# Performance work log

Measured on AMD Instinct MI355X. Metric: run time of the kernel, lower is better.

The kernel has to match this reference:

```python
import jax, jax.numpy as jnp
import numpy as np

B, LQ, E, R, H = 4, 64, 512, 32, 768
HOP = 2

def _linear(x, W, b):
    return x @ W + b

def setup_inputs() -> dict:
    key = jax.random.key(0)
    ks = jax.random.split(key, 20)
    s = 0.02
    inp = {
        'question_embedding': jax.random.normal(ks[0], (B, LQ, H), jnp.float32),
        'question_mask': jnp.ones((B, LQ), jnp.float32),
        'entity_embedding': jax.random.normal(ks[1], (B, E, H), jnp.float32),
        'rel_embedding': jax.random.normal(ks[2], (B, E, R, H), jnp.float32),
        'adj': jax.random.randint(ks[3], (B, E, R), 0, E, jnp.int32),
        'node_mask': jax.random.bernoulli(ks[4], 0.95, (B, E)).astype(jnp.float32),
        'adj_mask': jax.random.bernoulli(ks[5], 0.9, (B, E, R)).astype(jnp.float32),
        # params (Linear: y = x @ W + b, W is [in, out])
        'proj_W': jax.random.normal(ks[6], (H, H), jnp.float32) * s,
        'proj_b': jnp.zeros((H,), jnp.float32),
        'rproj_W': jax.random.normal(ks[7], (H, H), jnp.float32) * s,
        'rproj_b': jnp.zeros((H,), jnp.float32),
        'msg_W': jax.random.normal(ks[8], (HOP, 2 * H, H), jnp.float32) * s,
        'msg_b': jnp.zeros((HOP, H), jnp.float32),
        'upd_W': jax.random.normal(ks[9], (HOP, 2 * H, H), jnp.float32) * s,
        'upd_b': jnp.zeros((HOP, H), jnp.float32),
        'relscore_W': jax.random.normal(ks[10], (2 * H, 1), jnp.float32) * s,
        'relscore_b': jnp.zeros((1,), jnp.float32),
        'score_W': jax.random.normal(ks[11], (H, 1), jnp.float32) * s,
        'score_b': jnp.zeros((1,), jnp.float32),
    }
    return inp

def reference(question_embedding, question_mask, entity_embedding, rel_embedding,
              adj, node_mask, adj_mask,
              proj_W, proj_b, rproj_W, rproj_b, msg_W, msg_b, upd_W, upd_b,
              relscore_W, relscore_b, score_W, score_b):
    gelu = lambda x: jax.nn.gelu(x, approximate=False)  # torch nn.GELU default is erf
    dtype = rel_embedding.dtype
    NEG = jnp.finfo(dtype).min

    qe = _linear(question_embedding, proj_W, proj_b)          # [B,LQ,H]
    ee = _linear(entity_embedding, proj_W, proj_b)            # [B,E,H]
    re = _linear(rel_embedding, rproj_W, rproj_b)             # [B,E,R,H]

    qm = question_mask[..., None]
    q = jnp.sum(qe * qm, axis=1) / jnp.sum(qm, axis=1)        # [B,H]

    weight_mask = (1.0 - adj_mask) * NEG                      # [B,E,R]
    q_exp = jnp.broadcast_to(q[:, None, None, :], (B, E, R, H))
    weight_logit = (_linear(jnp.concatenate([re, q_exp], -1), relscore_W, relscore_b)
                    .squeeze(-1) + weight_mask)               # [B,E,R]
    weight = adj_mask * jax.nn.softmax(weight_logit, axis=-1) # [B,E,R]

    adj_flat = adj.reshape(B, E * R)
    for k in range(HOP):
        tail = jnp.take_along_axis(ee, adj_flat[:, :, None], axis=1).reshape(B, E, R, H)
        messages = gelu(_linear(jnp.concatenate([re, tail], -1), msg_W[k], msg_b[k]))
        agg = jnp.einsum('berh,ber->beh', messages, weight)
        ee = gelu(_linear(jnp.concatenate([ee, agg], -1), upd_W[k], upd_b[k]))

    node_neg = (1.0 - node_mask[..., None]) * NEG
    ent_score = (_linear(ee, score_W, score_b) + node_neg).squeeze(-1)  # [B,E]

    # triple_sim (computed under no_grad in torch)
    ee_c = jax.lax.stop_gradient(ee)
    q_c = jax.lax.stop_gradient(q)
    q_source = jnp.einsum('bh,beh->be', q_c, ee_c)            # source node e repeated over R
    q_source = jnp.broadcast_to(q_source[:, :, None], (B, E, R)).reshape(B, E * R)
    tail_final = jnp.take_along_axis(ee_c, adj_flat[:, :, None], axis=1)
    q_target = jnp.einsum('bh,bnh->bn', q_c, tail_final)      # [B,E*R]
    triple_sim = q_source + q_target + jax.lax.stop_gradient(weight_logit).reshape(B, E * R)

    return (ee, ent_score, weight_logit, triple_sim)
```

## Files before the change

### kernel.cpp

```cpp
#include <hip/hip_runtime.h>

#define NEGF (-3.0e38f)

#define BB 4
#define LQQ 64
#define EE_N 512
#define RR 32
#define HH 768

#define WS_QBAR 0
#define WS_Q    3072
#define WS_QD   6144
#define WS_WR1C 6656
#define WS_D0   7424
#define WS_D1   8192
#define WS_C0   8960
#define WS_C1   598784
#define WS_EEA  1188608
#define WS_EEB  2761472
#define WS_EEW  4334336
#define WS_W    5907200
#define WS_AGG  5972736
#define WS_SDOT 7545600
#define WS_CKT0 7547648
#define WS_CKT1 7842560
#define WS_PWT  8137472
#define WS_W0BT 8432384
#define WS_W1BT 8727296
#define WS_U0TT 9022208
#define WS_U0BT 9317120
#define WS_U1TT 9612032
#define WS_U1BT 9906944
#define WS_M0TT 10201856
#define WS_M1TT 10496768

typedef __attribute__((ext_vector_type(8))) short short8v;
typedef __attribute__((ext_vector_type(4))) short short4v;
typedef __attribute__((ext_vector_type(4))) float f32x4;

__device__ __forceinline__ float gelu_erf(float x) {
    return 0.5f * x * (1.0f + erff(x * 0.70710678118654752f));
}

__device__ __forceinline__ unsigned short f2bf(float f) {
    unsigned int u = __float_as_uint(f);
    unsigned int r = (u + 0x7fffu + ((u >> 16) & 1u)) >> 16;
    return (unsigned short)r;
}

__device__ __forceinline__ float bf2f(unsigned short h) {
    return __uint_as_float(((unsigned int)h) << 16);
}

__global__ void k_qbar(const float* __restrict__ QE, const float* __restrict__ QM,
                       float* __restrict__ qbar) {
    int b = blockIdx.x;
    int tid = threadIdx.x;
    float msum = 0.f;
    for (int l = 0; l < LQQ; ++l) msum += QM[b*LQQ + l];
    for (int h = tid; h < HH; h += 256) {
        float s = 0.f;
        for (int l = 0; l < LQQ; ++l)
            s += QM[b*LQQ + l] * QE[((size_t)(b*LQQ + l))*HH + h];
        qbar[b*HH + h] = s / msum;
    }
}

__global__ void k_small2(const float* __restrict__ RW, const float* __restrict__ RB,
                         const float* __restrict__ RSW, const float* __restrict__ RSB,
                         const float* __restrict__ q, float* __restrict__ wr1c,
                         float* __restrict__ qd) {
    const int wid = threadIdx.x >> 6, lane = threadIdx.x & 63;
    const int blk = blockIdx.x;
    if (blk < 192) {
        int row = blk*4 + wid;
        const float* a = RW + (size_t)row*HH;
        float acc = 0.f;
        #pragma unroll
        for (int p = 0; p < 3; ++p) {
            int i4 = (p*64 + lane) << 2;
            float4 x = *(const float4*)(a + i4);
            float4 w = *(const float4*)(RSW + i4);
            acc += x.x*w.x + x.y*w.y + x.z*w.z + x.w*w.w;
        }
        for (int off = 32; off; off >>= 1) acc += __shfl_xor(acc, off);
        if (lane == 0) wr1c[row] = acc;
    } else {
        float acc = 0.f, acc2 = 0.f;
        const float* src = q + wid*HH;
        #pragma unroll
        for (int p = 0; p < 3; ++p) {
            int i4 = (p*64 + lane) << 2;
            float4 x = *(const float4*)(src + i4);
            float4 w = *(const float4*)(RSW + HH + i4);
            acc += x.x*w.x + x.y*w.y + x.z*w.z + x.w*w.w;
            if (wid == 0) {
                float4 rb = *(const float4*)(RB + i4);
                float4 w0 = *(const float4*)(RSW + i4);
                acc2 += rb.x*w0.x + rb.y*w0.y + rb.z*w0.z + rb.w*w0.w;
            }
        }
        for (int off = 32; off; off >>= 1) { acc += __shfl_xor(acc, off); acc2 += __shfl_xor(acc2, off); }
        if (lane == 0) qd[wid] = acc;
        if (wid == 0 && lane == 0) qd[BB] = acc2 + RSB[0];
    }
}

__global__ void k_dk2(const unsigned short* __restrict__ M0tT,
                      const unsigned short* __restrict__ M1tT,
                      const float* __restrict__ RB, const float* __restrict__ MB,
                      float* __restrict__ d0, float* __restrict__ d1) {
    const int gw = blockIdx.x*4 + (threadIdx.x >> 6);
    const int lane = threadIdx.x & 63;
    const int hop = gw >= HH;
    const int n = hop ? gw - HH : gw;
    const unsigned short* row = (hop ? M1tT : M0tT) + (size_t)n*HH;
    float s = 0.f;
    #pragma unroll
    for (int p = 0; p < 3; ++p) {
        int i4 = (p*64 + lane) << 2;
        const unsigned short* hp = row + i4;
        float4 rv = *(const float4*)(RB + i4);
        s += bf2f(hp[0])*rv.x + bf2f(hp[1])*rv.y + bf2f(hp[2])*rv.z + bf2f(hp[3])*rv.w;
    }
    for (int off = 32; off; off >>= 1) s += __shfl_xor(s, off);
    if (lane == 0) (hop ? d1 : d0)[n] = s + MB[hop*HH + n];
}

__global__ __launch_bounds__(256) void gemm_f32(
    const float* __restrict__ A1, const float* __restrict__ W1,
    const float* __restrict__ bias, float* __restrict__ C,
    int M, int N, int K, int act)
{
    __shared__ float Asm[16][68];
    __shared__ float Bs[16][68];
    const int tid = threadIdx.x;
    const int n0 = blockIdx.x * 64;
    const int m0 = blockIdx.y * 64;
    const int tm = tid >> 4;
    const int tn = tid & 15;
    float acc[4][4] = {};
    for (int kk = 0; kk < K; kk += 16) {
        const int ar = tid >> 2;
        const int ak = (tid & 3) << 2;
        float4 av = make_float4(0.f, 0.f, 0.f, 0.f);
        if (m0 + ar < M) av = *(const float4*)(A1 + (size_t)(m0 + ar)*K + kk + ak);
        const int br = tid >> 4;
        const int bc = (tid & 15) << 2;
        float4 bv = *(const float4*)(W1 + (size_t)(kk + br)*N + n0 + bc);
        __syncthreads();
        Asm[ak+0][ar] = av.x; Asm[ak+1][ar] = av.y;
        Asm[ak+2][ar] = av.z; Asm[ak+3][ar] = av.w;
        *(float4*)&Bs[br][bc] = bv;
        __syncthreads();
        #pragma unroll
        for (int k = 0; k < 16; ++k) {
            float4 a4 = *(const float4*)&Asm[k][tm << 2];
            float4 b4 = *(const float4*)&Bs[k][tn << 2];
            float a[4] = {a4.x, a4.y, a4.z, a4.w};
            float b[4] = {b4.x, b4.y, b4.z, b4.w};
            #pragma unroll
            for (int i = 0; i < 4; ++i)
                #pragma unroll
                for (int j = 0; j < 4; ++j)
                    acc[i][j] = fmaf(a[i], b[j], acc[i][j]);
        }
    }
    float4 bb = make_float4(0.f, 0.f, 0.f, 0.f);
    if (bias) bb = *(const float4*)(bias + n0 + (tn << 2));
    float bbv[4] = {bb.x, bb.y, bb.z, bb.w};
    #pragma unroll
    for (int i = 0; i < 4; ++i) {
        int m = m0 + (tm << 2) + i;
        if (m >= M) break;
        #pragma unroll
        for (int j = 0; j < 4; ++j) {
            float v = acc[i][j] + bbv[j];
            if (act) v = gelu_erf(v);
            C[(size_t)m*N + n0 + (tn << 2) + j] = v;
        }
    }
}

__global__ void k_ckt(const float* __restrict__ Ck, unsigned short* __restrict__ CkT) {
    __shared__ float t[32][33];
    const int k0 = blockIdx.x * 32, n0 = blockIdx.y * 32;
    const int tid = threadIdx.x;
    {
        int r = tid >> 3;
        int c4 = (tid & 7) << 2;
        float4 v = *(const float4*)(Ck + (size_t)(k0 + r)*HH + n0 + c4);
        t[r][c4+0] = v.x; t[r][c4+1] = v.y; t[r][c4+2] = v.z; t[r][c4+3] = v.w;
    }
    __syncthreads();
    {
        int n = tid >> 3;
        int k4 = (tid & 7) << 2;
        unsigned short o[4];
        #pragma unroll
        for (int j = 0; j < 4; ++j) o[j] = f2bf(t[k4+j][n]);
        *(uint2*)(CkT + (size_t)(n0 + n)*HH + k0 + k4) = *(const uint2*)o;
    }
}

struct WPairs { const float* s[9]; unsigned short* d[9]; };
__global__ void k_w2bf(WPairs p) {
    __shared__ float t[32][33];
    const float* __restrict__ Ck = p.s[blockIdx.z];
    unsigned short* __restrict__ CkT = p.d[blockIdx.z];
    const int k0 = blockIdx.x * 32, n0 = blockIdx.y * 32;
    const int tid = threadIdx.x;
    {
        int r = tid >> 3;
        int c4 = (tid & 7) << 2;
        float4 v = *(const float4*)(Ck + (size_t)(k0 + r)*HH + n0 + c4);
        t[r][c4+0] = v.x; t[r][c4+1] = v.y; t[r][c4+2] = v.z; t[r][c4+3] = v.w;
    }
    __syncthreads();
    {
        int n = tid >> 3;
        int k4 = (tid & 7) << 2;
        unsigned short o[4];
        #pragma unroll
        for (int j = 0; j < 4; ++j) o[j] = f2bf(t[k4+j][n]);
        *(uint2*)(CkT + (size_t)(n0 + n)*HH + k0 + k4) = *(const uint2*)o;
    }
}

template<int BM>
__global__ __launch_bounds__(256) void gemm_bf16(
    const float* __restrict__ A1, const unsigned short* __restrict__ W1T,
    const float* __restrict__ A2, const unsigned short* __restrict__ W2T,
    const float* __restrict__ bias, float* __restrict__ C, int act)
{
    constexpr int FM = BM / 32;
    constexpr int AC = BM / 16;
    __shared__ alignas(16) unsigned short As[BM*64];
    __shared__ alignas(16) unsigned short Bs[128*64];
    const int tid = threadIdx.x;
    const int n0 = blockIdx.x * 128;
    const int m0 = blockIdx.y * BM;
    const int w = tid >> 6, lane = tid & 63;
    const int wm = w >> 1, wn = w & 1;
    const int l15 = lane & 15, l4 = lane >> 4;
    const int am_row = tid >> 4;
    const int am_col = (tid & 15) * 4;
    const int bm_row = tid >> 3;
    const int bm_col = (tid & 7) * 8;
    f32x4 acc[FM][4];
    #pragma unroll
    for (int i = 0; i < FM; ++i)
        #pragma unroll
        for (int j = 0; j < 4; ++j) acc[i][j] = (f32x4){0.f,0.f,0.f,0.f};
    const int nPass = (A2 != nullptr) ? 2 : 1;
    for (int pass = 0; pass < nPass; ++pass) {
        const float* __restrict__ A = pass ? A2 : A1;
        const unsigned short* __restrict__ WT = pass ? W2T : W1T;
        for (int k0 = 0; k0 < HH; k0 += 64) {
            float4 av[AC];
            #pragma unroll
            for (int c = 0; c < AC; ++c)
                av[c] = *(const float4*)(A + (size_t)(m0 + c*16 + am_row)*HH + k0 + am_col);
            short8v bv[4];
            #pragma unroll
            for (int i = 0; i < 4; ++i)
                bv[i] = *(const short8v*)(WT + (size_t)(n0 + i*32 + bm_row)*HH + k0 + bm_col);
            __syncthreads();
            #pragma unroll
            for (int c = 0; c < AC; ++c) {
                int r = c*16 + am_row;
                short4v h;
                h[0]=(short)f2bf(av[c].x); h[1]=(short)f2bf(av[c].y);
                h[2]=(short)f2bf(av[c].z); h[3]=(short)f2bf(av[c].w);
                int ba = r*128 + ((am_col*2) ^ ((r & 7) << 4));
                *(short4v*)&As[ba >> 1] = h;
            }
            #pragma unroll
            for (int i = 0; i < 4; ++i) {
                int r = i*32 + bm_row;
                int ba = r*128 + ((bm_col*2) ^ ((r & 7) << 4));
                *(short8v*)&Bs[ba >> 1] = bv[i];
            }
            __syncthreads();
            #pragma unroll
            for (int ks = 0; ks < 2; ++ks) {
                const int kb = ks*64 + l4*16;
                short8v af[FM], bf[4];
                #pragma unroll
                for (int fm = 0; fm < FM; ++fm) {
                    int row = wm*(FM*16) + fm*16 + l15;
                    af[fm] = *(const short8v*)&As[(row*128 + (kb ^ ((row & 7) << 4))) >> 1];
                }
                #pragma unroll
                for (int fn = 0; fn < 4; ++fn) {
                    int row = wn*64 + fn*16 + l15;
                    bf[fn] = *(const short8v*)&Bs[(row*128 + (kb ^ ((row & 7) << 4))) >> 1];
                }
                #pragma unroll
                for (int fm = 0; fm < FM; ++fm)
                    #pragma unroll
                    for (int fn = 0; fn < 4; ++fn)
                        acc[fm][fn] = __builtin_amdgcn_mfma_f32_16x16x32_bf16(af[fm], bf[fn], acc[fm][fn], 0, 0, 0);
            }
            __syncthreads();
        }
    }
    #pragma unroll
    for (int fn = 0; fn < 4; ++fn) {
        int col = n0 + wn*64 + fn*16 + l15;
        float bb = bias ? bias[col] : 0.f;
        #pragma unroll
        for (int fm = 0; fm < FM; ++fm) {
            int row0 = m0 + wm*(FM*16) + fm*16 + l4*4;
            #pragma unroll
            for (int j = 0; j < 4; ++j) {
                float v = acc[fm][fn][j] + bb;
                if (act) v = gelu_erf(v);
                C[(size_t)(row0 + j)*HH + col] = v;
            }
        }
    }
}

template<int FUSE>
__global__ __launch_bounds__(256, 3) void k_msg6(
    const float* __restrict__ rel, const unsigned short* __restrict__ CkT,
    const float* __restrict__ dk, const float* __restrict__ eeW,
    const float* __restrict__ weight_in, const int* __restrict__ adj,
    const float* __restrict__ wr1c, const float* __restrict__ qd,
    const float* __restrict__ am,
    float* __restrict__ agg, float* __restrict__ logit_out,
    float* __restrict__ weight_out)
{
    __shared__ alignas(16) unsigned short As[64*64];
    __shared__ alignas(16) unsigned short Bs[256*64];
    int*   adjS = (int*)As;
    float* wS   = (float*)(As + 128);
    float* lgS  = (float*)(As + 256);
    const int tid = threadIdx.x;
    const int bid = blockIdx.x;
    const int L = (bid & 7) * 384 + (bid >> 3);
    const int mt = L / 3, nt = L - mt*3;
    const int n0 = nt * 256;
    const int m0 = mt * 64;
    const int be0 = mt * 2;
    const int b = be0 >> 9;
    const int wn = tid >> 6, lane = tid & 63;
    const int l15 = lane & 15, l4 = lane >> 4;
    const int am_row = tid >> 4;
    const int am_col = (tid & 15) * 4;
    const int bm_row = tid >> 3;
    const int bm_col = (tid & 7) * 8;
    const float* apA = rel + (size_t)(m0 + am_row)*HH + am_col;
    const unsigned short* apB = CkT + (size_t)(n0 + bm_row)*HH + bm_col;

    f32x4 acc[4][4];
    #pragma unroll
    for (int i = 0; i < 4; ++i)
        #pragma unroll
        for (int j = 0; j < 4; ++j) acc[i][j] = (f32x4){0.f,0.f,0.f,0.f};
    float lg[4] = {0.f, 0.f, 0.f, 0.f};

    float4 av[4];
    short8v bv[8];
    #pragma unroll
    for (int c = 0; c < 4; ++c) av[c] = *(const float4*)(apA + (size_t)c*16*HH);
    #pragma unroll
    for (int i = 0; i < 8; ++i) bv[i] = *(const short8v*)(apB + (size_t)i*32*HH);

    for (int t = 0; t < 12; ++t) {
        const int k0 = t*64;
        #pragma unroll
        for (int c = 0; c < 4; ++c) {
            int r = c*16 + am_row;
            short4v h;
            h[0]=(short)f2bf(av[c].x); h[1]=(short)f2bf(av[c].y);
            h[2]=(short)f2bf(av[c].z); h[3]=(short)f2bf(av[c].w);
            int ba = r*128 + ((am_col*2) ^ ((r & 7) << 4));
            *(short4v*)&As[ba >> 1] = h;
        }
        #pragma unroll
        for (int i = 0; i < 8; ++i) {
            int r = i*32 + bm_row;
            int ba = r*128 + ((bm_col*2) ^ ((r & 7) << 4));
            *(short8v*)&Bs[ba >> 1] = bv[i];
        }
        if (FUSE) {
            float4 wv = *(const float4*)(wr1c + k0 + am_col);
            #pragma unroll
            for (int c = 0; c < 4; ++c)
                lg[c] += av[c].x*wv.x + av[c].y*wv.y + av[c].z*wv.z + av[c].w*wv.w;
        }
        if (t < 11) {
            #pragma unroll
            for (int c = 0; c < 4; ++c)
                av[c] = *(const float4*)(apA + (size_t)c*16*HH + k0 + 64);
            #pragma unroll
            for (int i = 0; i < 8; ++i)
                bv[i] = *(const short8v*)(apB + (size_t)i*32*HH + k0 + 64);
        }
        __syncthreads();
        #pragma unroll
        for (int ks = 0; ks < 2; ++ks) {
            const int kb = ks*64 + l4*16;
            short8v af[4], bf[4];
            #pragma unroll
            for (int fm = 0; fm < 4; ++fm) {
                int row = fm*16 + l15;
                af[fm] = *(const short8v*)&As[(row*128 + (kb ^ ((row & 7) << 4))) >> 1];
            }
            #pragma unroll
            for (int fn = 0; fn < 4; ++fn) {
                int row = wn*64 + fn*16 + l15;
                bf[fn] = *(const short8v*)&Bs[(row*128 + (kb ^ ((row & 7) << 4))) >> 1];
            }
            #pragma unroll
            for (int fm = 0; fm < 4; ++fm)
                #pragma unroll
                for (int fn = 0; fn < 4; ++fn)
                    acc[fm][fn] = __builtin_amdgcn_mfma_f32_16x16x32_bf16(af[fm], bf[fn], acc[fm][fn], 0, 0, 0);
        }
        __syncthreads();
    }
    if (tid < 64) adjS[tid] = adj[be0*RR + tid];
    if (!FUSE && tid < 64) wS[tid] = weight_in[be0*RR + tid];

    if (FUSE) {
        #pragma unroll
        for (int c = 0; c < 4; ++c) {
            lg[c] += __shfl_xor(lg[c], 1);
            lg[c] += __shfl_xor(lg[c], 2);
            lg[c] += __shfl_xor(lg[c], 4);
            lg[c] += __shfl_xor(lg[c], 8);
        }
        if ((tid & 15) == 0) {
            #pragma unroll
            for (int c = 0; c < 4; ++c) lgS[c*16 + am_row] = lg[c];
        }
        __syncthreads();
        if (tid < 64) {
            int r = tid & 31;
            float amv = am[be0*RR + tid];
            float l = lgS[tid] + qd[b] + qd[BB] + (1.0f - amv) * NEGF;
            float mx = l;
            #pragma unroll
            for (int off = 16; off; off >>= 1) mx = fmaxf(mx, __shfl_xor(mx, off, 32));
            float e = expf(l - mx);
            float sm = e;
            #pragma unroll
            for (int off = 16; off; off >>= 1) sm += __shfl_xor(sm, off, 32);
            float wgt = amv * e / sm;
            wS[tid] = wgt;
            if (nt == 0) {
                logit_out[be0*RR + tid] = l;
                weight_out[be0*RR + tid] = wgt;
            }
            (void)r;
        }
    }
    __syncthreads();

    #pragma unroll
    for (int eh = 0; eh < 2; ++eh) {
        const int be = be0 + eh;
        #pragma unroll
        for (int fn = 0; fn < 4; ++fn) {
            int col = n0 + wn*64 + fn*16 + l15;
            float d = dk[col];
            float s = 0.f;
            #pragma unroll
            for (int fp = 0; fp < 2; ++fp) {
                const int fm = eh*2 + fp;
                #pragma unroll
                for (int j = 0; j < 4; ++j) {
                    int rr = fp*16 + l4*4 + j;
                    int t = adjS[eh*RR + rr];
                    float tail = eeW[((size_t)(b*EE_N + t))*HH + col];
                    s += wS[eh*RR + rr] * gelu_erf(acc[fm][fn][j] + tail + d);
                }
            }
            s += __shfl_xor(s, 16);
            s += __shfl_xor(s, 32);
            if (l4 == 0) agg[(size_t)be*HH + col] = s;
        }
    }
}

__global__ __launch_bounds__(256) void k_score(const float* __restrict__ ee,
                                               const float* __restrict__ SW,
                                               const float* __restrict__ SB,
                                               const float* __restrict__ NM,
                                               const float* __restrict__ q,
                                               float* __restrict__ score,
                                               float* __restrict__ sdot) {
    const int wid = threadIdx.x >> 6, lane = threadIdx.x & 63;
    const int row = blockIdx.x*4 + wid;
    const int b = row >> 9;
    const float* er = ee + (size_t)row*HH;
    const float* qr = q + b*HH;
    float a1 = 0.f, a2 = 0.f;
    #pragma unroll
    for (int p = 0; p < 3; ++p) {
        int i4 = (p*64 + lane) << 2;
        float4 e4 = *(const float4*)(er + i4);
        float4 s4 = *(const float4*)(SW + i4);
        float4 q4 = *(const float4*)(qr + i4);
        a1 += e4.x*s4.x + e4.y*s4.y + e4.z*s4.z + e4.w*s4.w;
        a2 += e4.x*q4.x + e4.y*q4.y + e4.z*q4.z + e4.w*q4.w;
    }
    for (int off = 32; off; off >>= 1) { a1 += __shfl_xor(a1, off); a2 += __shfl_xor(a2, off); }
    if (lane == 0) {
        score[row] = a1 + SB[0] + (1.0f - NM[row]) * NEGF;
        sdot[row] = a2;
    }
}

__global__ void k_triple(const float* __restrict__ sdot, const int* __restrict__ adj,
                         const float* __restrict__ logit, float* __restrict__ tri) {
    int idx = blockIdx.x*256 + threadIdx.x;
    int b = idx >> 14;
    int n = idx & 16383;
    int e = n >> 5;
    int a = adj[idx];
    tri[idx] = sdot[b*EE_N + e] + sdot[b*EE_N + a] + logit[idx];
}

extern "C" void kernel_launch(void* const* d_in, const int* in_sizes, int n_in,
                              void* d_out, int out_size, void* d_ws, size_t ws_size,
                              hipStream_t stream) {
    const float* QE  = (const float*)d_in[0];
    const float* QM  = (const float*)d_in[1];
    const float* ENT = (const float*)d_in[2];
    const float* REL = (const float*)d_in[3];
    const int*   ADJ = (const int*)d_in[4];
    const float* NM  = (const float*)d_in[5];
    const float* AM  = (const float*)d_in[6];
    const float* PW  = (const float*)d_in[7];
    const float* PB  = (const float*)d_in[8];
    const float* RW  = (const float*)d_in[9];
    const float* RB  = (const float*)d_in[10];
    const float* MW  = (const float*)d_in[11];
    const float* MB  = (const float*)d_in[12];
    const float* UW  = (const float*)d_in[13];
    const float* UB  = (const float*)d_in[14];
    const float* RSW = (const float*)d_in[15];
    const float* RSB = (const float*)d_in[16];
    const float* SW  = (const float*)d_in[17];
    const float* SB  = (const float*)d_in[18];

    float* out = (float*)d_out;
    float* ws  = (float*)d_ws;
    float* o_ee    = out;
    float* o_score = out + 1572864;
    float* o_logit = out + 1574912;
    float* o_tri   = out + 1640448;

    unsigned short* CkT0 = (unsigned short*)(ws + WS_CKT0);
    unsigned short* CkT1 = (unsigned short*)(ws + WS_CKT1);
    unsigned short* PWT  = (unsigned short*)(ws + WS_PWT);
    unsigned short* W0bT = (unsigned short*)(ws + WS_W0BT);
    unsigned short* W1bT = (unsigned short*)(ws + WS_W1BT);
    unsigned short* U0tT = (unsigned short*)(ws + WS_U0TT);
    unsigned short* U0bT = (unsigned short*)(ws + WS_U0BT);
    unsigned short* U1tT = (unsigned short*)(ws + WS_U1TT);
    unsigned short* U1bT = (unsigned short*)(ws + WS_U1BT);
    unsigned short* M0tT = (unsigned short*)(ws + WS_M0TT);
    unsigned short* M1tT = (unsigned short*)(ws + WS_M1TT);

    const size_t HT = (size_t)2*HH*HH;
    const size_t BOT = (size_t)HH*HH;

    k_qbar<<<BB, 256, 0, stream>>>(QE, QM, ws + WS_QBAR);
    gemm_f32<<<dim3(12,1), 256, 0, stream>>>(ws + WS_QBAR, PW, PB, ws + WS_Q, BB, HH, HH, 0);
    k_small2<<<193, 256, 0, stream>>>(RW, RB, RSW, RSB, ws + WS_Q, ws + WS_WR1C, ws + WS_QD);

    WPairs wp;
    wp.s[0] = PW;            wp.d[0] = PWT;
    wp.s[1] = MW + BOT;      wp.d[1] = W0bT;
    wp.s[2] = MW + HT + BOT; wp.d[2] = W1bT;
    wp.s[3] = UW;            wp.d[3] = U0tT;
    wp.s[4] = UW + BOT;      wp.d[4] = U0bT;
    wp.s[5] = UW + HT;       wp.d[5] = U1tT;
    wp.s[6] = UW + HT + BOT; wp.d[6] = U1bT;
    wp.s[7] = MW;            wp.d[7] = M0tT;
    wp.s[8] = MW + HT;       wp.d[8] = M1tT;
    k_w2bf<<<dim3(24,24,9), 256, 0, stream>>>(wp);

    k_dk2<<<384, 256, 0, stream>>>(M0tT, M1tT, RB, MB, ws + WS_D0, ws + WS_D1);

    gemm_bf16<32><<<dim3(6,24), 256, 0, stream>>>(RW, M0tT, nullptr, nullptr, nullptr,
                                                  ws + WS_C0, 0);
    gemm_bf16<32><<<dim3(6,24), 256, 0, stream>>>(RW, M1tT, nullptr, nullptr, nullptr,
                                                  ws + WS_C1, 0);
    k_ckt<<<dim3(24,24), 256, 0, stream>>>(ws + WS_C0, CkT0);
    k_ckt<<<dim3(24,24), 256, 0, stream>>>(ws + WS_C1, CkT1);

    gemm_bf16<32><<<dim3(6,64), 256, 0, stream>>>(ENT, PWT, nullptr, nullptr, PB,
                                                  ws + WS_EEA, 0);

    gemm_bf16<32><<<dim3(6,64), 256, 0, stream>>>(ws + WS_EEA, W0bT, nullptr, nullptr, nullptr,
                                                  ws + WS_EEW, 0);
    k_msg6<1><<<3072, 256, 0, stream>>>(REL, CkT0, ws + WS_D0, ws + WS_EEW,
                                        nullptr, ADJ, ws + WS_WR1C, ws + WS_QD, AM,
                                        ws + WS_AGG, o_logit, ws + WS_W);
    gemm_bf16<32><<<dim3(6,64), 256, 0, stream>>>(ws + WS_EEA, U0tT, ws + WS_AGG, U0bT, UB,
                                                  ws + WS_EEB, 1);

    gemm_bf16<32><<<dim3(6,64), 256, 0, stream>>>(ws + WS_EEB, W1bT, nullptr, nullptr, nullptr,
                                                  ws + WS_EEW, 0);
    k_msg6<0><<<3072, 256, 0, stream>>>(REL, CkT1, ws + WS_D1, ws + WS_EEW,
                                        ws + WS_W, ADJ, ws + WS_WR1C, ws + WS_QD, AM,
                                        ws + WS_AGG, nullptr, nullptr);
    gemm_bf16<32><<<dim3(6,64), 256, 0, stream>>>(ws + WS_EEB, U1tT, ws + WS_AGG, U1bT,
                                                  UB + HH, o_ee, 1);

    k_score<<<512, 256, 0, stream>>>(o_ee, SW, SB, NM, ws + WS_Q, o_score, ws + WS_SDOT);
    k_triple<<<256, 256, 0, stream>>>(ws + WS_SDOT, ADJ, o_logit, o_tri);
}
```

Before: 529.5 us.

## Pre-convert relation embeddings to bf16 once and stream via direct-to-LDS loads

Adds a conversion pass that writes rel_embedding as bf16 into workspace and computes the relation-score logits there, followed by a separate softmax kernel. Both message hops then read the half-size bf16 copy through global_load_lds into a 128x128 tile, instead of each re-reading and converting the fp32 tensor. This trades one full fp32 read plus a bf16 write for halved traffic in the two hops. It only runs when the workspace is large enough, otherwise the old path is kept.

```diff
diff --git a/kernel.cpp b/kernel.cpp
--- a/kernel.cpp
+++ b/kernel.cpp
@@ -33,10 +33,16 @@
 #define WS_U1BT 9906944
 #define WS_M0TT 10201856
 #define WS_M1TT 10496768
+#define WS_RELBF 10791680
+#define WS_NEED_BYTES 143830016ull
 
 typedef __attribute__((ext_vector_type(8))) short short8v;
 typedef __attribute__((ext_vector_type(4))) short short4v;
 typedef __attribute__((ext_vector_type(4))) float f32x4;
+
+#define GLOAD_LDS16(gp, lp) __builtin_amdgcn_global_load_lds( \
+    (const __attribute__((address_space(1))) void*)(gp), \
+    (__attribute__((address_space(3))) void*)(lp), 16, 0, 0)
 
 __device__ __forceinline__ float gelu_erf(float x) {
     return 0.5f * x * (1.0f + erff(x * 0.70710678118654752f));
@@ -227,6 +233,46 @@
     }
 }
 
+__global__ __launch_bounds__(256) void k_cvt(
+    const float* __restrict__ rel, const float* __restrict__ wr1c,
+    const float* __restrict__ qd, const float* __restrict__ am,
+    unsigned short* __restrict__ relbf, float* __restrict__ logit) {
+    const int wid = threadIdx.x >> 6, lane = threadIdx.x & 63;
+    const long row = (long)blockIdx.x*4 + wid;
+    const float* a = rel + row*HH;
+    unsigned short* o = relbf + row*HH;
+    float acc = 0.f;
+    #pragma unroll
+    for (int p = 0; p < 3; ++p) {
+        int i4 = (p*64 + lane) << 2;
+        float4 x = *(const float4*)(a + i4);
+        float4 wv = *(const float4*)(wr1c + i4);
+        acc += x.x*wv.x + x.y*wv.y + x.z*wv.z + x.w*wv.w;
+        unsigned short h[4] = {f2bf(x.x), f2bf(x.y), f2bf(x.z), f2bf(x.w)};
+        *(uint2*)(o + i4) = *(const uint2*)h;
+    }
+    for (int off = 32; off; off >>= 1) acc += __shfl_xor(acc, off);
+    if (lane == 0) {
+        int b = (int)(row >> 14);
+        logit[row] = acc + qd[b] + qd[BB] + (1.0f - am[row]) * NEGF;
+    }
+}
+
+__global__ void k_softmax(const float* __restrict__ logit, const float* __restrict__ am,
+                          float* __restrict__ weight) {
+    int row = blockIdx.x;
+    int lane = threadIdx.x;
+    if (lane < 32) {
+        float l = logit[row*RR + lane];
+        float m = l;
+        for (int off = 16; off; off >>= 1) m = fmaxf(m, __shfl_xor(m, off, 32));
+        float e = expf(l - m);
+        float s = e;
+        for (int off = 16; off; off >>= 1) s += __shfl_xor(s, off, 32);
+        weight[row*RR + lane] = am[row*RR + lane] * e / s;
+    }
+}
+
 template<int BM>
 __global__ __launch_bounds__(256) void gemm_bf16(
     const float* __restrict__ A1, const unsigned short* __restrict__ W1T,
@@ -318,6 +364,102 @@
                 if (act) v = gelu_erf(v);
                 C[(size_t)(row0 + j)*HH + col] = v;
             }
+        }
+    }
+}
+
+__global__ __launch_bounds__(256, 3) void k_msg7(
+    const unsigned short* __restrict__ relbf, const unsigned short* __restrict__ CkT,
+    const float* __restrict__ dk, const float* __restrict__ eeW,
+    const float* __restrict__ weight, const int* __restrict__ adj,
+    float* __restrict__ agg)
+{
+    __shared__ alignas(16) unsigned short As[128*64];
+    __shared__ alignas(16) unsigned short Bs[128*64];
+    __shared__ int   adjS[4][RR];
+    __shared__ float wS[4][RR];
+    const int tid = threadIdx.x;
+    const int bid = blockIdx.x;
+    const int L = (bid & 7) * 384 + (bid >> 3);
+    const int mt = L / 6, nt = L - mt*6;
+    const int n0 = nt * 128;
+    const int m0 = mt * 128;
+    const int be0 = mt * 4;
+    const int b = be0 >> 9;
+    if (tid < 128) {
+        int el = tid >> 5, r = tid & 31;
+        adjS[el][r] = adj[(be0 + el)*RR + r];
+        wS[el][r]   = weight[(be0 + el)*RR + r];
+    }
+    const int w = tid >> 6, lane = tid & 63;
+    const int wm = w >> 1, wn = w & 1;
+    const int l15 = lane & 15, l4 = lane >> 4;
+    const int crow = lane >> 3;
+    const int ce   = (lane & 7) * 8;
+
+    f32x4 acc[4][4];
+    #pragma unroll
+    for (int i = 0; i < 4; ++i)
+        #pragma unroll
+        for (int j = 0; j < 4; ++j) acc[i][j] = (f32x4){0.f,0.f,0.f,0.f};
+
+    for (int t = 0; t < 12; ++t) {
+        const int k0 = t*64;
+        #pragma unroll
+        for (int c = 0; c < 4; ++c) {
+            int rbase = w*32 + c*8;
+            GLOAD_LDS16(relbf + (size_t)(m0 + rbase + crow)*HH + k0 + ce,
+                        &As[rbase*64]);
+            GLOAD_LDS16(CkT   + (size_t)(n0 + rbase + crow)*HH + k0 + ce,
+                        &Bs[rbase*64]);
+        }
+        __syncthreads();
+        #pragma unroll
+        for (int ks = 0; ks < 2; ++ks) {
+            const int ko = ks*32 + l4*8;
+            short8v af[4], bf[4];
+            #pragma unroll
+            for (int fm = 0; fm < 4; ++fm) {
+                int row = wm*64 + fm*16 + l15;
+                af[fm] = *(const short8v*)&As[row*64 + ko];
+            }
+            #pragma unroll
+            for (int fn = 0; fn < 4; ++fn) {
+                int row = wn*64 + fn*16 + l15;
+                bf[fn] = *(const short8v*)&Bs[row*64 + ko];
+            }
+            #pragma unroll
+            for (int fm = 0; fm < 4; ++fm)
+                #pragma unroll
+                for (int fn = 0; fn < 4; ++fn)
+                    acc[fm][fn] = __builtin_amdgcn_mfma_f32_16x16x32_bf16(af[fm], bf[fn], acc[fm][fn], 0, 0, 0);
+        }
+        __syncthreads();
+    }
+
+    #pragma unroll
+    for (int eh = 0; eh < 2; ++eh) {
+        const int el = wm*2 + eh;
+        const int be = be0 + el;
+        #pragma unroll
+        for (int fn = 0; fn < 4; ++fn) {
+            int col = n0 + wn*64 + fn*16 + l15;
+            float d = dk[col];
+            float s = 0.f;
+            #pragma unroll
+            for (int fp = 0; fp < 2; ++fp) {
+                const int fm = eh*2 + fp;
+                #pragma unroll
+                for (int j = 0; j < 4; ++j) {
+                    int rr = fp*16 + l4*4 + j;
+                    int tl = adjS[el][rr];
+                    float tail = eeW[((size_t)(b*EE_N + tl))*HH + col];
+                    s += wS[el][rr] * gelu_erf(acc[fm][fn][j] + tail + d);
+                }
+            }
+            s += __shfl_xor(s, 16);
+            s += __shfl_xor(s, 32);
+            if (l4 == 0) agg[(size_t)be*HH + col] = s;
         }
     }
 }
@@ -353,21 +495,18 @@
     const int bm_col = (tid & 7) * 8;
     const float* apA = rel + (size_t)(m0 + am_row)*HH + am_col;
     const unsigned short* apB = CkT + (size_t)(n0 + bm_row)*HH + bm_col;
-
     f32x4 acc[4][4];
     #pragma unroll
     for (int i = 0; i < 4; ++i)
         #pragma unroll
         for (int j = 0; j < 4; ++j) acc[i][j] = (f32x4){0.f,0.f,0.f,0.f};
     float lg[4] = {0.f, 0.f, 0.f, 0.f};
-
     float4 av[4];
     short8v bv[8];
     #pragma unroll
     for (int c = 0; c < 4; ++c) av[c] = *(const float4*)(apA + (size_t)c*16*HH);
     #pragma unroll
     for (int i = 0; i < 8; ++i) bv[i] = *(const short8v*)(apB + (size_t)i*32*HH);
-
     for (int t = 0; t < 12; ++t) {
         const int k0 = t*64;
         #pragma unroll
@@ -424,7 +563,6 @@
     }
     if (tid < 64) adjS[tid] = adj[be0*RR + tid];
     if (!FUSE && tid < 64) wS[tid] = weight_in[be0*RR + tid];
-
     if (FUSE) {
         #pragma unroll
         for (int c = 0; c < 4; ++c) {
@@ -439,7 +577,6 @@
         }
         __syncthreads();
         if (tid < 64) {
-            int r = tid & 31;
             float amv = am[be0*RR + tid];
             float l = lgS[tid] + qd[b] + qd[BB] + (1.0f - amv) * NEGF;
             float mx = l;
@@ -455,11 +592,9 @@
                 logit_out[be0*RR + tid] = l;
                 weight_out[be0*RR + tid] = wgt;
             }
-            (void)r;
         }
     }
     __syncthreads();
-
     #pragma unroll
     for (int eh = 0; eh < 2; ++eh) {
         const int be = be0 + eh;
@@ -474,8 +609,8 @@
                 #pragma unroll
                 for (int j = 0; j < 4; ++j) {
                     int rr = fp*16 + l4*4 + j;
-                    int t = adjS[eh*RR + rr];
-                    float tail = eeW[((size_t)(b*EE_N + t))*HH + col];
+                    int tl = adjS[eh*RR + rr];
+                    float tail = eeW[((size_t)(b*EE_N + tl))*HH + col];
                     s += wS[eh*RR + rr] * gelu_erf(acc[fm][fn][j] + tail + d);
                 }
             }
@@ -566,6 +701,9 @@
     unsigned short* U1bT = (unsigned short*)(ws + WS_U1BT);
     unsigned short* M0tT = (unsigned short*)(ws + WS_M0TT);
     unsigned short* M1tT = (unsigned short*)(ws + WS_M1TT);
+    unsigned short* RELBF = (unsigned short*)(ws + WS_RELBF);
+
+    const bool big = ws_size >= WS_NEED_BYTES;
 
     const size_t HT = (size_t)2*HH*HH;
     const size_t BOT = (size_t)HH*HH;
@@ -598,21 +736,39 @@
     gemm_bf16<32><<<dim3(6,64), 256, 0, stream>>>(ENT, PWT, nullptr, nullptr, PB,
                                                   ws + WS_EEA, 0);
 
-    gemm_bf16<32><<<dim3(6,64), 256, 0, stream>>>(ws + WS_EEA, W0bT, nullptr, nullptr, nullptr,
-                                                  ws + WS_EEW, 0);
-    k_msg6<1><<<3072, 256, 0, stream>>>(REL, CkT0, ws + WS_D0, ws + WS_EEW,
-                                        nullptr, ADJ, ws + WS_WR1C, ws + WS_QD, AM,
-                                        ws + WS_AGG, o_logit, ws + WS_W);
-    gemm_bf16<32><<<dim3(6,64), 256, 0, stream>>>(ws + WS_EEA, U0tT, ws + WS_AGG, U0bT, UB,
-                                                  ws + WS_EEB, 1);
-
-    gemm_bf16<32><<<dim3(6,64), 256, 0, stream>>>(ws + WS_EEB, W1bT, nullptr, nullptr, nullptr,
-                                                  ws + WS_EEW, 0);
-    k_msg6<0><<<3072, 256, 0, stream>>>(REL, CkT1, ws + WS_D1, ws + WS_EEW,
-                                        ws + WS_W, ADJ, ws + WS_WR1C, ws + WS_QD, AM,
-                                        ws + WS_AGG, nullptr, nullptr);
-    gemm_bf16<32><<<dim3(6,64), 256, 0, stream>>>(ws + WS_EEB, U1tT, ws + WS_AGG, U1bT,
-                                                  UB + HH, o_ee, 1);
+    if (big) {
+        k_cvt<<<16384, 256, 0, stream>>>(REL, ws + WS_WR1C, ws + WS_QD, AM,
+                                         RELBF, o_logit);
+        k_softmax<<<2048, 64, 0, stream>>>(o_logit, AM, ws + WS_W);
+
+        gemm_bf16<32><<<dim3(6,64), 256, 0, stream>>>(ws + WS_EEA, W0bT, nullptr, nullptr, nullptr,
+                                                      ws + WS_EEW, 0);
+        k_msg7<<<3072, 256, 0, stream>>>(RELBF, CkT0, ws + WS_D0, ws + WS_EEW,
+                                         ws + WS_W, ADJ, ws + WS_AGG);
+        gemm_bf16<32><<<dim3(6,64), 256, 0, stream>>>(ws + WS_EEA, U0tT, ws + WS_AGG, U0bT, UB,
+                                                      ws + WS_EEB, 1);
+        gemm_bf16<32><<<dim3(6,64), 256, 0, stream>>>(ws + WS_EEB, W1bT, nullptr, nullptr, nullptr,
+                                                      ws + WS_EEW, 0);
+        k_msg7<<<3072, 256, 0, stream>>>(RELBF, CkT1, ws + WS_D1, ws + WS_EEW,
+                                         ws + WS_W, ADJ, ws + WS_AGG);
+        gemm_bf16<32><<<dim3(6,64), 256, 0, stream>>>(ws + WS_EEB, U1tT, ws + WS_AGG, U1bT,
+                                                      UB + HH, o_ee, 1);
+    } else {
+        gemm_bf16<32><<<dim3(6,64), 256, 0, stream>>>(ws + WS_EEA, W0bT, nullptr, nullptr, nullptr,
+                                                      ws + WS_EEW, 0);
+        k_msg6<1><<<3072, 256, 0, stream>>>(REL, CkT0, ws + WS_D0, ws + WS_EEW,
+                                            nullptr, ADJ, ws + WS_WR1C, ws + WS_QD, AM,
+                                            ws + WS_AGG, o_logit, ws + WS_W);
+        gemm_bf16<32><<<dim3(6,64), 256, 0, stream>>>(ws + WS_EEA, U0tT, ws + WS_AGG, U0bT, UB,
+                                                      ws + WS_EEB, 1);
+        gemm_bf16<32><<<dim3(6,64), 256, 0, stream>>>(ws + WS_EEB, W1bT, nullptr, nullptr, nullptr,
+                                                      ws + WS_EEW, 0);
+        k_msg6<0><<<3072, 256, 0, stream>>>(REL, CkT1, ws + WS_D1, ws + WS_EEW,
+                                            ws + WS_W, ADJ, ws + WS_WR1C, ws + WS_QD, AM,
+                                            ws + WS_AGG, nullptr, nullptr);
+        gemm_bf16<32><<<dim3(6,64), 256, 0, stream>>>(ws + WS_EEB, U1tT, ws + WS_AGG, U1bT,
+                                                      UB + HH, o_ee, 1);
+    }
 
     k_score<<<512, 256, 0, stream>>>(o_ee, SW, SB, NM, ws + WS_Q, o_score, ws + WS_SDOT);
     k_triple<<<256, 256, 0, stream>>>(ws + WS_SDOT, ADJ, o_logit, o_tri);
```

Measured after the change: 585.5 us. 1.11x slower.
